# Performance work log

Hardware: AMD Instinct MI355X
Metric: run time of the kernel (lower is better)

Reference implementation:

```python
import jax, jax.numpy as jnp
import numpy as np

D, H, WIN, OUT = 3, 64, 8, 32
B, T = 128, 129
IU, JU = np.triu_indices(D, k=1)  # Lyndon pairs i<j at depth 2


def setup_inputs() -> dict:
    key = jax.random.key(0)
    ks = jax.random.split(key, 10)
    ts = jnp.broadcast_to(jnp.linspace(0.0, 1.0, T), (B, T))
    # path-like control values: cumulative sum of small increments
    x = jnp.cumsum(0.1 * jax.random.normal(ks[0], (B, T, D)), axis=1)
    def lin(k, o, i):
        return jax.random.normal(k, (o, i), dtype=jnp.float32) * (1.0 / np.sqrt(i))
    return {
        "ts": ts, "x": x,
        "W0": lin(ks[1], 128, D), "b0": jnp.zeros((128,), jnp.float32),
        "W1": lin(ks[2], 128, 128), "b1": jnp.zeros((128,), jnp.float32),
        "W2": lin(ks[3], H, 128), "b2": jnp.zeros((H,), jnp.float32),
        "V0": lin(ks[4], 128, H), "c0": jnp.zeros((128,), jnp.float32),
        "V1": lin(ks[5], 128, 128), "c1": jnp.zeros((128,), jnp.float32),
        "V2": lin(ks[6], D * H, 128), "c2": jnp.zeros((D * H,), jnp.float32),
        "R": lin(ks[7], OUT, H), "rb": jnp.zeros((OUT,), jnp.float32),
    }


def reference(ts, x, W0, b0, W1, b1, W2, b2, V0, c0, V1, c1, V2, c2, R, rb):
    sp = jax.nn.softplus

    def init_mlp(v):  # R^D -> R^H, Euclidean retract = identity
        return W2 @ sp(W1 @ sp(W0 @ v + b0) + b1) + b2

    def vf_flat(y):  # R^H -> R^{D*H}, final tanh (split_multi_vector_field)
        return jnp.tanh(V2 @ sp(V1 @ sp(V0 @ y + c0) + c1) + c2)

    def F(y):
        # level-1 fields f_i(y) as rows of m: (D, H)
        m = vf_flat(y).reshape(D, H)
        # J[a, b] = D f_b(y) . f_a(y)  via JVPs in directions f_a
        J = jax.vmap(lambda v: jax.jvp(vf_flat, (y,), (v,))[1].reshape(D, H))(m)
        # Lyndon level-2 brackets [f_i, f_j] = Df_j.f_i - Df_i.f_j
        br = J[IU, JU] - J[JU, IU]  # (D*(D-1)/2, H)
        return jnp.concatenate([m, br], axis=0).T  # (H, logsig_size)

    def logsigs_fn(xs):  # depth-2 log-signatures over disjoint windows
        nw = (T - 1) // WIN
        idx = (np.arange(nw) * WIN)[:, None] + np.arange(WIN + 1)[None, :]
        win = xs[idx]
        lvl1 = win[:, -1] - win[:, 0]       # increments
        rel = win[:, :-1] - win[:, :1]      # path relative to window start
        dv = win[:, 1:] - win[:, :-1]       # increments within window
        a = jnp.einsum('nki,nkj->nij', rel, dv)
        area = 0.5 * (a - jnp.swapaxes(a, 1, 2))  # Levy areas
        return jnp.concatenate([lvl1, area[:, IU, JU]], axis=1)

    def solve_one(t, xs):
        h0 = init_mlp(xs[0])
        ls = logsigs_fn(xs)                       # (nw, L)
        t_sig = t[::WIN]                          # window knot times
        slopes = ls / (t_sig[1:] - t_sig[:-1])[:, None]  # dz/dt per window
        slope_steps = jnp.repeat(slopes, WIN, axis=0)    # (T-1, L)
        dts = t[1:] - t[:-1]

        def step(y, inp):  # Heun integration of dy = F(y) dz/dt dt
            dt, s = inp
            k1 = F(y) @ s
            k2 = F(y + dt * k1) @ s
            yn = y + 0.5 * dt * (k1 + k2)
            return yn, yn

        _, ys = jax.lax.scan(step, h0, (dts, slope_steps))
        hidden = jnp.concatenate([h0[None], ys], axis=0)  # (T, H)
        return jnp.tanh(hidden @ R.T + rb)                # evolving readout

    return jax.vmap(solve_one)(ts, x)  # (B, T, OUT)
```

## Files before the change

### kernel.cpp

```cpp
#include <hip/hip_runtime.h>
#include <math.h>

#define BB 128
#define TT 129
#define NSTEP 128
#define NW 16
#define WINW 8
#define OUTD 32

typedef _Float16 h2_t __attribute__((ext_vector_type(2)));

__device__ __forceinline__ float fast_rcp(float v){ return __builtin_amdgcn_rcpf(v); }
__device__ __forceinline__ float tanh_f(float v){
    float ax=fminf(fabsf(v),15.f); float e=__expf(2.f*ax);
    float r=1.f-2.f*fast_rcp(e+1.f); return copysignf(r,v);
}
__device__ __forceinline__ void sigsp(float z, float& sp, float& sig){
    float e  = __expf(-fabsf(z));
    float rc = fast_rcp(1.f+e);
    sp  = fmaxf(z,0.f) + __logf(1.f+e);
    sig = (z>=0.f) ? rc : e*rc;
}
__device__ __forceinline__ float pack2(float a,float b){
    h2_t h; h.x=(_Float16)a; h.y=(_Float16)b; return __builtin_bit_cast(float,h);
}
__device__ __forceinline__ float dot2c(float wc,float ac,float acc){
    return __builtin_amdgcn_fdot2(__builtin_bit_cast(h2_t,wc),__builtin_bit_cast(h2_t,ac),acc,false);
}
__device__ __forceinline__ float dot2q(float4 wq,float4 aq,float acc){
    acc=dot2c(wq.x,aq.x,acc); acc=dot2c(wq.y,aq.y,acc);
    acc=dot2c(wq.z,aq.z,acc); acc=dot2c(wq.w,aq.w,acc); return acc;
}
#define DOT4(acc,Wv,Av) acc += (Wv).x*(Av).x + (Wv).y*(Av).y + (Wv).z*(Av).z + (Wv).w*(Av).w
#define PIN4(v) asm volatile("" : "+v"((v).x), "+v"((v).y), "+v"((v).z), "+v"((v).w))

#define DPPF(x,ctrl) __builtin_bit_cast(float, __builtin_amdgcn_update_dpp(0, __builtin_bit_cast(int,(x)), (ctrl), 0xF, 0xF, true))
__device__ __forceinline__ float dpp_xor1(float x){ return DPPF(x,0xB1); }
__device__ __forceinline__ float dpp_xor2(float x){ return DPPF(x,0x4E); }
__device__ __forceinline__ float dpp_hmir(float x){ return DPPF(x,0x141); }
#define RED4(x) do{ x += dpp_xor1(x); x += dpp_xor2(x); }while(0)

__global__ __launch_bounds__(512, 1)
void ncde_solve(const float* __restrict__ ts, const float* __restrict__ x,
                const float* __restrict__ W0, const float* __restrict__ b0,
                const float* __restrict__ W1, const float* __restrict__ b1,
                const float* __restrict__ W2, const float* __restrict__ b2,
                const float* __restrict__ V0, const float* __restrict__ c0,
                const float* __restrict__ V1, const float* __restrict__ c1,
                const float* __restrict__ V2, const float* __restrict__ c2,
                const float* __restrict__ R, const float* __restrict__ rb,
                float* __restrict__ out)
{
    const int b = blockIdx.x;
    const int t = threadIdx.x;
    const int r = t >> 2, q = t & 3;
    const int rl = r & 63;
    const int pt = (t >= 256) ? (t - 256) : 0;
    const int prow = pt >> 3, poct = pt & 7;

    __shared__ __align__(16) float RSh[OUTD*68];
    __shared__ __align__(16) float ySh[64];
    __shared__ __align__(16) float yp[32], y2p[32];
    __shared__ __align__(16) float a0H[64], a1H[64];
    __shared__ __align__(16) float mpH[96];
    __shared__ __align__(16) float u0H[192], wH[192];
    __shared__ float mF32[64];
    __shared__ float slopesSh[NW][6];
    __shared__ float dtsSh[NSTEP];

    float4 v0c[2], v1c[4], v2c[3][4];
    {
        auto pkld = [](const float* src)->float4{
            const float4* p=(const float4*)src;
            float4 a=p[0], c=p[1];
            float4 rr; rr.x=pack2(a.x,a.y); rr.y=pack2(a.z,a.w); rr.z=pack2(c.x,c.y); rr.w=pack2(c.z,c.w);
            return rr;
        };
        {
            const float* base = V0 + r*64 + q*16;
            v0c[0]=pkld(base); v0c[1]=pkld(base+8);
        }
        {
            const float* base = V1 + r*128 + q*32;
            #pragma unroll
            for (int k=0;k<4;k++) v1c[k]=pkld(base+8*k);
        }
        #pragma unroll
        for (int i=0;i<3;i++){
            const float* base = V2 + (rl+64*i)*128 + q*32;
            #pragma unroll
            for (int k=0;k<4;k++) v2c[i][k]=pkld(base+8*k);
        }
        PIN4(v0c[0]); PIN4(v0c[1]);
        #pragma unroll
        for (int k=0;k<4;k++) PIN4(v1c[k]);
        #pragma unroll
        for (int i=0;i<3;i++){
            #pragma unroll
            for (int k=0;k<4;k++) PIN4(v2c[i][k]);
        }
    }
    const float c0r=c0[r], c1r=c1[r];
    const float c2a=c2[rl], c2b=c2[64+rl], c2c=c2[128+rl];
    const float rbp = rb[prow & 31];

    for (int i=t; i<OUTD*64; i+=512) RSh[(i>>6)*68 + (i&63)] = R[i];
    const float* tsb = ts + (size_t)b*TT;
    if (t < NSTEP) dtsSh[t] = tsb[t+1] - tsb[t];

    if (t < NW) {
        const int w = t;
        const float* xs = x + (size_t)(b*TT + w*WINW)*3;
        float x0c[3] = {xs[0], xs[1], xs[2]};
        float prev[3] = {x0c[0], x0c[1], x0c[2]};
        float am01=0.f, am02=0.f, am12=0.f, am10=0.f, am20=0.f, am21=0.f;
        #pragma unroll
        for (int k=0;k<WINW;k++) {
            float cur[3] = {xs[(k+1)*3+0], xs[(k+1)*3+1], xs[(k+1)*3+2]};
            float rel[3], dv[3];
            #pragma unroll
            for (int c=0;c<3;c++){ rel[c]=prev[c]-x0c[c]; dv[c]=cur[c]-prev[c]; }
            am01 += rel[0]*dv[1]; am10 += rel[1]*dv[0];
            am02 += rel[0]*dv[2]; am20 += rel[2]*dv[0];
            am12 += rel[1]*dv[2]; am21 += rel[2]*dv[1];
            prev[0]=cur[0]; prev[1]=cur[1]; prev[2]=cur[2];
        }
        const float invden = 1.f/(tsb[(w+1)*WINW] - tsb[w*WINW]);
        slopesSh[w][0] = (prev[0]-x0c[0])*invden;
        slopesSh[w][1] = (prev[1]-x0c[1])*invden;
        slopesSh[w][2] = (prev[2]-x0c[2])*invden;
        slopesSh[w][3] = 0.5f*(am01-am10)*invden;
        slopesSh[w][4] = 0.5f*(am02-am20)*invden;
        slopesSh[w][5] = 0.5f*(am12-am21)*invden;
    }

    if (t < 128) {
        const float xv0 = x[(size_t)b*TT*3+0];
        const float xv1 = x[(size_t)b*TT*3+1];
        const float xv2 = x[(size_t)b*TT*3+2];
        float acc = b0[t] + W0[t*3]*xv0 + W0[t*3+1]*xv1 + W0[t*3+2]*xv2;
        float sp, sg; sigsp(acc, sp, sg);
        u0H[t] = sp;
    }
    __syncthreads();
    if (t < 128) {
        float acc = b1[t];
        const float4* rw = (const float4*)(W1 + t*128);
        #pragma unroll 8
        for (int k=0;k<32;k++){ float4 wv=rw[k]; float4 av=*(const float4*)&u0H[4*k]; DOT4(acc,wv,av); }
        float sp, sg; sigsp(acc, sp, sg);
        wH[t] = sp;
    }
    __syncthreads();
    if (t < 64) {
        float acc = b2[t];
        const float4* rw = (const float4*)(W2 + t*128);
        #pragma unroll 8
        for (int k=0;k<32;k++){ float4 wv=rw[k]; float4 av=*(const float4*)&wH[4*k]; DOT4(acc,wv,av); }
        ySh[t] = acc;
        ((_Float16*)yp)[t] = (_Float16)acc;
    }
    __syncthreads();

    float yreg = (r < 64) ? ySh[r] : 0.f;
    float k1r = 0.f;
    float S0,S1,S2,S3,S4,S5;

    auto Feval = [&](const float* ypIn, bool first, float dtc) {
        float sig0r, sig1r, mA=0.f, mC=0.f;
        {
            const float4* Y = (const float4*)ypIn;
            float za = dot2q(v0c[0], Y[q*2], 0.f);
            float zb = dot2q(v0c[1], Y[q*2+1], 0.f);
            float z = za + zb;
            RED4(z); z += c0r;
            float sp; sigsp(z, sp, sig0r);
            if (!q) ((_Float16*)a0H)[r] = (_Float16)sp;
        }
        __syncthreads();
        {
            const float4* A = (const float4*)a0H + q*4;
            float za = dot2q(v1c[0], A[0], 0.f); za = dot2q(v1c[1], A[1], za);
            float zb = dot2q(v1c[2], A[2], 0.f); zb = dot2q(v1c[3], A[3], zb);
            float z = za + zb;
            RED4(z); z += c1r;
            float sp; sigsp(z, sp, sig1r);
            if (!q) ((_Float16*)a1H)[r] = (_Float16)sp;
        }
        __syncthreads();
        {
            const float4* A = (const float4*)a1H + q*4;
            float4 a0=A[0],a1=A[1],a2=A[2],a3=A[3];
            if (r < 64){
                float zAa=dot2q(v2c[0][0],a0,0.f); zAa=dot2q(v2c[0][1],a1,zAa);
                float zAb=dot2q(v2c[0][2],a2,0.f); zAb=dot2q(v2c[0][3],a3,zAb);
                float zCa=dot2q(v2c[2][0],a0,0.f); zCa=dot2q(v2c[2][1],a1,zCa);
                float zCb=dot2q(v2c[2][2],a2,0.f); zCb=dot2q(v2c[2][3],a3,zCb);
                float zA=zAa+zAb, zC=zCa+zCb;
                RED4(zA); RED4(zC);
                mA = tanh_f(zA + c2a); mC = tanh_f(zC + c2c);
                if (!q){
                    ((_Float16*)mpH)[rl]     = (_Float16)mA;
                    ((_Float16*)mpH)[128+rl] = (_Float16)mC;
                }
            } else {
                float zBa=dot2q(v2c[1][0],a0,0.f); zBa=dot2q(v2c[1][1],a1,zBa);
                float zBb=dot2q(v2c[1][2],a2,0.f); zBb=dot2q(v2c[1][3],a3,zBb);
                float zB=zBa+zBb;
                RED4(zB);
                float mB = tanh_f(zB + c2b);
                if (!q){
                    ((_Float16*)mpH)[64+rl] = (_Float16)mB;
                    mF32[rl] = mB;
                }
            }
        }
        __syncthreads();
        {
            const float4* M = (const float4*)mpH;
            float4 g0a=M[q*2],    g0b=M[q*2+1];
            float4 g1a=M[8+q*2],  g1b=M[8+q*2+1];
            float4 g2a=M[16+q*2], g2b=M[16+q*2+1];
            float t0=dot2q(v0c[0],g0a,0.f); t0=dot2q(v0c[1],g0b,t0);
            float t1=dot2q(v0c[0],g1a,0.f); t1=dot2q(v0c[1],g1b,t1);
            float t2=dot2q(v0c[0],g2a,0.f); t2=dot2q(v0c[1],g2b,t2);
            RED4(t0); RED4(t1); RED4(t2);
            if (!q){
                ((_Float16*)u0H)[r]     = (_Float16)(sig0r*t0);
                ((_Float16*)u0H)[128+r] = (_Float16)(sig0r*t1);
                ((_Float16*)u0H)[256+r] = (_Float16)(sig0r*t2);
            }
        }
        __syncthreads();
        {
            const float4* U = (const float4*)u0H;
            float t0a=0.f,t0b=0.f,t1a=0.f,t1b=0.f,t2a=0.f,t2b=0.f;
            #pragma unroll
            for (int k=0;k<2;k++){
                float4 w = v1c[k];
                t0a=dot2q(w,U[q*4+k],t0a); t1a=dot2q(w,U[16+q*4+k],t1a); t2a=dot2q(w,U[32+q*4+k],t2a);
            }
            #pragma unroll
            for (int k=2;k<4;k++){
                float4 w = v1c[k];
                t0b=dot2q(w,U[q*4+k],t0b); t1b=dot2q(w,U[16+q*4+k],t1b); t2b=dot2q(w,U[32+q*4+k],t2b);
            }
            float t0=t0a+t0b, t1=t1a+t1b, t2=t2a+t2b;
            RED4(t0); RED4(t1); RED4(t2);
            if (!q){
                float w0 = sig1r*(S3*t1 + S4*t2);
                float w1 = sig1r*(S3*t0 - S5*t2);
                float w2 = sig1r*(S4*t0 + S5*t1);
                ((_Float16*)wH)[r]     = (_Float16)w0;
                ((_Float16*)wH)[128+r] = (_Float16)w1;
                ((_Float16*)wH)[256+r] = (_Float16)w2;
            }
        }
        __syncthreads();
        if (r < 64){
            const float4* W = (const float4*)wH;
            float D0a=dot2q(v2c[0][0],W[q*4+0],0.f);   D0a=dot2q(v2c[0][1],W[q*4+1],D0a);
            float D0b=dot2q(v2c[0][2],W[q*4+2],0.f);   D0b=dot2q(v2c[0][3],W[q*4+3],D0b);
            float D1a=dot2q(v2c[1][0],W[16+q*4+0],0.f);D1a=dot2q(v2c[1][1],W[16+q*4+1],D1a);
            float D1b=dot2q(v2c[1][2],W[16+q*4+2],0.f);D1b=dot2q(v2c[1][3],W[16+q*4+3],D1b);
            float D2a=dot2q(v2c[2][0],W[32+q*4+0],0.f);D2a=dot2q(v2c[2][1],W[32+q*4+1],D2a);
            float D2b=dot2q(v2c[2][2],W[32+q*4+2],0.f);D2b=dot2q(v2c[2][3],W[32+q*4+3],D2b);
            float D0=D0a+D0b, D1=D1a+D1b, D2=D2a+D2b;
            RED4(D0); RED4(D1); RED4(D2);
            const float mB = mF32[rl];
            const float dtA = 1.f-mA*mA, dtB = 1.f-mB*mB, dtC = 1.f-mC*mC;
            float kk = mA*S0 + mB*S1 + mC*S2 - dtA*D0 + dtB*D1 + dtC*D2;
            if (first){
                k1r = kk;
                float y2 = yreg + dtc*kk;
                if (!q) ((_Float16*)y2p)[rl] = (_Float16)y2;
            } else {
                yreg += 0.5f*dtc*(k1r + kk);
                if (!q){ ((_Float16*)yp)[rl] = (_Float16)yreg; ySh[rl] = yreg; }
            }
        }
        __syncthreads();
    };

    auto proj = [&](int stp) {
        if (t >= 256){
            const float4* rr = (const float4*)(RSh + prow*68 + poct*8);
            const float4* yy = (const float4*)(ySh + poct*8);
            float pacc = 0.f;
            DOT4(pacc, rr[0], yy[0]); DOT4(pacc, rr[1], yy[1]);
            pacc += dpp_xor1(pacc);
            pacc += dpp_xor2(pacc);
            pacc += dpp_hmir(pacc);
            if (!poct) out[(size_t)(b*TT + stp)*OUTD + prow] = tanh_f(pacc + rbp);
        }
    };

    for (int step=0; step<NSTEP; ++step) {
        proj(step);
        const int w = step >> 3;
        S0=slopesSh[w][0]; S1=slopesSh[w][1]; S2=slopesSh[w][2];
        S3=slopesSh[w][3]; S4=slopesSh[w][4]; S5=slopesSh[w][5];
        const float dtc = dtsSh[step];
        Feval(yp,  true,  dtc);
        Feval(y2p, false, dtc);
    }
    proj(NSTEP);
}

extern "C" void kernel_launch(void* const* d_in, const int* in_sizes, int n_in,
                              void* d_out, int out_size, void* d_ws, size_t ws_size,
                              hipStream_t stream) {
    const float* ts = (const float*)d_in[0];
    const float* x  = (const float*)d_in[1];
    const float* W0 = (const float*)d_in[2];
    const float* b0 = (const float*)d_in[3];
    const float* W1 = (const float*)d_in[4];
    const float* b1 = (const float*)d_in[5];
    const float* W2 = (const float*)d_in[6];
    const float* b2 = (const float*)d_in[7];
    const float* V0 = (const float*)d_in[8];
    const float* c0 = (const float*)d_in[9];
    const float* V1 = (const float*)d_in[10];
    const float* c1 = (const float*)d_in[11];
    const float* V2 = (const float*)d_in[12];
    const float* c2 = (const float*)d_in[13];
    const float* R  = (const float*)d_in[14];
    const float* rb = (const float*)d_in[15];
    float* out = (float*)d_out;

    ncde_solve<<<dim3(BB), dim3(512), 0, stream>>>(
        ts, x, W0, b0, W1, b1, W2, b2, V0, c0, V1, c1, V2, c2, R, rb, out);
}
```

Baseline: 590.9 us.

## Halve block to 256 threads, each quad computing two hidden rows

Shrinks each block from 512 to 256 threads. Each 4-lane group now owns two rows of the 128-wide layers and all three rows of the output layer, so the weight slices kept in registers double. The goal is to drop the idle half-block branches in the output and JVP stages and to make the many per-step barriers cheaper with fewer waves to synchronise. The cost is more register pressure and more serial dot-product work per thread, with only 128 blocks on the device.

```diff
diff --git a/kernel.cpp b/kernel.cpp
--- a/kernel.cpp
+++ b/kernel.cpp
@@ -40,7 +40,7 @@
 __device__ __forceinline__ float dpp_hmir(float x){ return DPPF(x,0x141); }
 #define RED4(x) do{ x += dpp_xor1(x); x += dpp_xor2(x); }while(0)
 
-__global__ __launch_bounds__(512, 1)
+__global__ __launch_bounds__(256, 1)
 void ncde_solve(const float* __restrict__ ts, const float* __restrict__ x,
                 const float* __restrict__ W0, const float* __restrict__ b0,
                 const float* __restrict__ W1, const float* __restrict__ b1,
@@ -54,9 +54,7 @@
     const int b = blockIdx.x;
     const int t = threadIdx.x;
     const int r = t >> 2, q = t & 3;
-    const int rl = r & 63;
-    const int pt = (t >= 256) ? (t - 256) : 0;
-    const int prow = pt >> 3, poct = pt & 7;
+    const int prow = t >> 3, poct = t & 7;
 
     __shared__ __align__(16) float RSh[OUTD*68];
     __shared__ __align__(16) float ySh[64];
@@ -64,11 +62,10 @@
     __shared__ __align__(16) float a0H[64], a1H[64];
     __shared__ __align__(16) float mpH[96];
     __shared__ __align__(16) float u0H[192], wH[192];
-    __shared__ float mF32[64];
     __shared__ float slopesSh[NW][6];
     __shared__ float dtsSh[NSTEP];
 
-    float4 v0c[2], v1c[4], v2c[3][4];
+    float4 v0c[2][2], v1c[2][4], v2c[3][4];
     {
         auto pkld = [](const float* src)->float4{
             const float4* p=(const float4*)src;
@@ -76,35 +73,42 @@
             float4 rr; rr.x=pack2(a.x,a.y); rr.y=pack2(a.z,a.w); rr.z=pack2(c.x,c.y); rr.w=pack2(c.z,c.w);
             return rr;
         };
-        {
-            const float* base = V0 + r*64 + q*16;
-            v0c[0]=pkld(base); v0c[1]=pkld(base+8);
-        }
-        {
-            const float* base = V1 + r*128 + q*32;
-            #pragma unroll
-            for (int k=0;k<4;k++) v1c[k]=pkld(base+8*k);
+        #pragma unroll
+        for (int i=0;i<2;i++){
+            const float* base = V0 + (r+64*i)*64 + q*16;
+            v0c[i][0]=pkld(base); v0c[i][1]=pkld(base+8);
+        }
+        #pragma unroll
+        for (int i=0;i<2;i++){
+            const float* base = V1 + (r+64*i)*128 + q*32;
+            #pragma unroll
+            for (int k=0;k<4;k++) v1c[i][k]=pkld(base+8*k);
         }
         #pragma unroll
         for (int i=0;i<3;i++){
-            const float* base = V2 + (rl+64*i)*128 + q*32;
+            const float* base = V2 + (r+64*i)*128 + q*32;
             #pragma unroll
             for (int k=0;k<4;k++) v2c[i][k]=pkld(base+8*k);
         }
-        PIN4(v0c[0]); PIN4(v0c[1]);
-        #pragma unroll
-        for (int k=0;k<4;k++) PIN4(v1c[k]);
+        #pragma unroll
+        for (int i=0;i<2;i++){ PIN4(v0c[i][0]); PIN4(v0c[i][1]); }
+        #pragma unroll
+        for (int i=0;i<2;i++){
+            #pragma unroll
+            for (int k=0;k<4;k++) PIN4(v1c[i][k]);
+        }
         #pragma unroll
         for (int i=0;i<3;i++){
             #pragma unroll
             for (int k=0;k<4;k++) PIN4(v2c[i][k]);
         }
     }
-    const float c0r=c0[r], c1r=c1[r];
-    const float c2a=c2[rl], c2b=c2[64+rl], c2c=c2[128+rl];
+    const float c0A=c0[r], c0B=c0[64+r];
+    const float c1A=c1[r], c1B=c1[64+r];
+    const float c2a=c2[r], c2b=c2[64+r], c2c=c2[128+r];
     const float rbp = rb[prow & 31];
 
-    for (int i=t; i<OUTD*64; i+=512) RSh[(i>>6)*68 + (i&63)] = R[i];
+    for (int i=t; i<OUTD*64; i+=256) RSh[(i>>6)*68 + (i&63)] = R[i];
     const float* tsb = ts + (size_t)b*TT;
     if (t < NSTEP) dtsSh[t] = tsb[t+1] - tsb[t];
 
@@ -162,57 +166,62 @@
     }
     __syncthreads();
 
-    float yreg = (r < 64) ? ySh[r] : 0.f;
+    float yreg = ySh[r];
     float k1r = 0.f;
     float S0,S1,S2,S3,S4,S5;
 
     auto Feval = [&](const float* ypIn, bool first, float dtc) {
-        float sig0r, sig1r, mA=0.f, mC=0.f;
+        float sig0A,sig0B,sig1A,sig1B,mA,mB,mC,dtA,dtB,dtC;
         {
             const float4* Y = (const float4*)ypIn;
-            float za = dot2q(v0c[0], Y[q*2], 0.f);
-            float zb = dot2q(v0c[1], Y[q*2+1], 0.f);
-            float z = za + zb;
-            RED4(z); z += c0r;
-            float sp; sigsp(z, sp, sig0r);
-            if (!q) ((_Float16*)a0H)[r] = (_Float16)sp;
+            float4 y0=Y[q*2], y1=Y[q*2+1];
+            float zA = dot2q(v0c[0][0],y0,0.f); zA = dot2q(v0c[0][1],y1,zA);
+            float zB = dot2q(v0c[1][0],y0,0.f); zB = dot2q(v0c[1][1],y1,zB);
+            RED4(zA); RED4(zB);
+            zA += c0A; zB += c0B;
+            float spA, spB;
+            sigsp(zA, spA, sig0A); sigsp(zB, spB, sig0B);
+            if (!q){
+                ((_Float16*)a0H)[r]    = (_Float16)spA;
+                ((_Float16*)a0H)[64+r] = (_Float16)spB;
+            }
         }
         __syncthreads();
         {
             const float4* A = (const float4*)a0H + q*4;
-            float za = dot2q(v1c[0], A[0], 0.f); za = dot2q(v1c[1], A[1], za);
-            float zb = dot2q(v1c[2], A[2], 0.f); zb = dot2q(v1c[3], A[3], zb);
-            float z = za + zb;
-            RED4(z); z += c1r;
-            float sp; sigsp(z, sp, sig1r);
-            if (!q) ((_Float16*)a1H)[r] = (_Float16)sp;
+            float4 a0=A[0],a1=A[1],a2=A[2],a3=A[3];
+            float zAa=dot2q(v1c[0][0],a0,0.f); zAa=dot2q(v1c[0][1],a1,zAa);
+            float zAb=dot2q(v1c[0][2],a2,0.f); zAb=dot2q(v1c[0][3],a3,zAb);
+            float zBa=dot2q(v1c[1][0],a0,0.f); zBa=dot2q(v1c[1][1],a1,zBa);
+            float zBb=dot2q(v1c[1][2],a2,0.f); zBb=dot2q(v1c[1][3],a3,zBb);
+            float zA=zAa+zAb, zB=zBa+zBb;
+            RED4(zA); RED4(zB);
+            zA += c1A; zB += c1B;
+            float spA, spB;
+            sigsp(zA, spA, sig1A); sigsp(zB, spB, sig1B);
+            if (!q){
+                ((_Float16*)a1H)[r]    = (_Float16)spA;
+                ((_Float16*)a1H)[64+r] = (_Float16)spB;
+            }
         }
         __syncthreads();
         {
             const float4* A = (const float4*)a1H + q*4;
             float4 a0=A[0],a1=A[1],a2=A[2],a3=A[3];
-            if (r < 64){
-                float zAa=dot2q(v2c[0][0],a0,0.f); zAa=dot2q(v2c[0][1],a1,zAa);
-                float zAb=dot2q(v2c[0][2],a2,0.f); zAb=dot2q(v2c[0][3],a3,zAb);
-                float zCa=dot2q(v2c[2][0],a0,0.f); zCa=dot2q(v2c[2][1],a1,zCa);
-                float zCb=dot2q(v2c[2][2],a2,0.f); zCb=dot2q(v2c[2][3],a3,zCb);
-                float zA=zAa+zAb, zC=zCa+zCb;
-                RED4(zA); RED4(zC);
-                mA = tanh_f(zA + c2a); mC = tanh_f(zC + c2c);
-                if (!q){
-                    ((_Float16*)mpH)[rl]     = (_Float16)mA;
-                    ((_Float16*)mpH)[128+rl] = (_Float16)mC;
-                }
-            } else {
-                float zBa=dot2q(v2c[1][0],a0,0.f); zBa=dot2q(v2c[1][1],a1,zBa);
-                float zBb=dot2q(v2c[1][2],a2,0.f); zBb=dot2q(v2c[1][3],a3,zBb);
-                float zB=zBa+zBb;
-                RED4(zB);
-                float mB = tanh_f(zB + c2b);
-                if (!q){
-                    ((_Float16*)mpH)[64+rl] = (_Float16)mB;
-                    mF32[rl] = mB;
-                }
+            float zAa=dot2q(v2c[0][0],a0,0.f); zAa=dot2q(v2c[0][1],a1,zAa);
+            float zAb=dot2q(v2c[0][2],a2,0.f); zAb=dot2q(v2c[0][3],a3,zAb);
+            float zBa=dot2q(v2c[1][0],a0,0.f); zBa=dot2q(v2c[1][1],a1,zBa);
+            float zBb=dot2q(v2c[1][2],a2,0.f); zBb=dot2q(v2c[1][3],a3,zBb);
+            float zCa=dot2q(v2c[2][0],a0,0.f); zCa=dot2q(v2c[2][1],a1,zCa);
+            float zCb=dot2q(v2c[2][2],a2,0.f); zCb=dot2q(v2c[2][3],a3,zCb);
+            float zA=zAa+zAb, zB=zBa+zBb, zC=zCa+zCb;
+            RED4(zA); RED4(zB); RED4(zC);
+            mA=tanh_f(zA+c2a); mB=tanh_f(zB+c2b); mC=tanh_f(zC+c2c);
+            dtA=1.f-mA*mA; dtB=1.f-mB*mB; dtC=1.f-mC*mC;
+            if (!q){
+                ((_Float16*)mpH)[r]     = (_Float16)mA;
+                ((_Float16*)mpH)[64+r]  = (_Float16)mB;
+                ((_Float16*)mpH)[128+r] = (_Float16)mC;
             }
         }
         __syncthreads();
@@ -221,43 +230,57 @@
             float4 g0a=M[q*2],    g0b=M[q*2+1];
             float4 g1a=M[8+q*2],  g1b=M[8+q*2+1];
             float4 g2a=M[16+q*2], g2b=M[16+q*2+1];
-            float t0=dot2q(v0c[0],g0a,0.f); t0=dot2q(v0c[1],g0b,t0);
-            float t1=dot2q(v0c[0],g1a,0.f); t1=dot2q(v0c[1],g1b,t1);
-            float t2=dot2q(v0c[0],g2a,0.f); t2=dot2q(v0c[1],g2b,t2);
-            RED4(t0); RED4(t1); RED4(t2);
-            if (!q){
-                ((_Float16*)u0H)[r]     = (_Float16)(sig0r*t0);
-                ((_Float16*)u0H)[128+r] = (_Float16)(sig0r*t1);
-                ((_Float16*)u0H)[256+r] = (_Float16)(sig0r*t2);
+            float t0A=dot2q(v0c[0][0],g0a,0.f); t0A=dot2q(v0c[0][1],g0b,t0A);
+            float t1A=dot2q(v0c[0][0],g1a,0.f); t1A=dot2q(v0c[0][1],g1b,t1A);
+            float t2A=dot2q(v0c[0][0],g2a,0.f); t2A=dot2q(v0c[0][1],g2b,t2A);
+            float t0B=dot2q(v0c[1][0],g0a,0.f); t0B=dot2q(v0c[1][1],g0b,t0B);
+            float t1B=dot2q(v0c[1][0],g1a,0.f); t1B=dot2q(v0c[1][1],g1b,t1B);
+            float t2B=dot2q(v0c[1][0],g2a,0.f); t2B=dot2q(v0c[1][1],g2b,t2B);
+            RED4(t0A); RED4(t1A); RED4(t2A);
+            RED4(t0B); RED4(t1B); RED4(t2B);
+            if (!q){
+                ((_Float16*)u0H)[r]      = (_Float16)(sig0A*t0A);
+                ((_Float16*)u0H)[64+r]   = (_Float16)(sig0B*t0B);
+                ((_Float16*)u0H)[128+r]  = (_Float16)(sig0A*t1A);
+                ((_Float16*)u0H)[192+r]  = (_Float16)(sig0B*t1B);
+                ((_Float16*)u0H)[256+r]  = (_Float16)(sig0A*t2A);
+                ((_Float16*)u0H)[320+r]  = (_Float16)(sig0B*t2B);
             }
         }
         __syncthreads();
         {
             const float4* U = (const float4*)u0H;
-            float t0a=0.f,t0b=0.f,t1a=0.f,t1b=0.f,t2a=0.f,t2b=0.f;
+            float t0Aa=0.f,t0Ab=0.f,t1Aa=0.f,t1Ab=0.f,t2Aa=0.f,t2Ab=0.f;
+            float t0Ba=0.f,t0Bb=0.f,t1Ba=0.f,t1Bb=0.f,t2Ba=0.f,t2Bb=0.f;
             #pragma unroll
             for (int k=0;k<2;k++){
-                float4 w = v1c[k];
-                t0a=dot2q(w,U[q*4+k],t0a); t1a=dot2q(w,U[16+q*4+k],t1a); t2a=dot2q(w,U[32+q*4+k],t2a);
+                float4 wa=v1c[0][k], wb=v1c[1][k];
+                float4 g0=U[q*4+k], g1=U[16+q*4+k], g2=U[32+q*4+k];
+                t0Aa=dot2q(wa,g0,t0Aa); t1Aa=dot2q(wa,g1,t1Aa); t2Aa=dot2q(wa,g2,t2Aa);
+                t0Ba=dot2q(wb,g0,t0Ba); t1Ba=dot2q(wb,g1,t1Ba); t2Ba=dot2q(wb,g2,t2Ba);
             }
             #pragma unroll
             for (int k=2;k<4;k++){
-                float4 w = v1c[k];
-                t0b=dot2q(w,U[q*4+k],t0b); t1b=dot2q(w,U[16+q*4+k],t1b); t2b=dot2q(w,U[32+q*4+k],t2b);
-            }
-            float t0=t0a+t0b, t1=t1a+t1b, t2=t2a+t2b;
-            RED4(t0); RED4(t1); RED4(t2);
-            if (!q){
-                float w0 = sig1r*(S3*t1 + S4*t2);
-                float w1 = sig1r*(S3*t0 - S5*t2);
-                float w2 = sig1r*(S4*t0 + S5*t1);
-                ((_Float16*)wH)[r]     = (_Float16)w0;
-                ((_Float16*)wH)[128+r] = (_Float16)w1;
-                ((_Float16*)wH)[256+r] = (_Float16)w2;
-            }
-        }
-        __syncthreads();
-        if (r < 64){
+                float4 wa=v1c[0][k], wb=v1c[1][k];
+                float4 g0=U[q*4+k], g1=U[16+q*4+k], g2=U[32+q*4+k];
+                t0Ab=dot2q(wa,g0,t0Ab); t1Ab=dot2q(wa,g1,t1Ab); t2Ab=dot2q(wa,g2,t2Ab);
+                t0Bb=dot2q(wb,g0,t0Bb); t1Bb=dot2q(wb,g1,t1Bb); t2Bb=dot2q(wb,g2,t2Bb);
+            }
+            float t0A=t0Aa+t0Ab, t1A=t1Aa+t1Ab, t2A=t2Aa+t2Ab;
+            float t0B=t0Ba+t0Bb, t1B=t1Ba+t1Bb, t2B=t2Ba+t2Bb;
+            RED4(t0A); RED4(t1A); RED4(t2A);
+            RED4(t0B); RED4(t1B); RED4(t2B);
+            if (!q){
+                ((_Float16*)wH)[r]      = (_Float16)(sig1A*(S3*t1A + S4*t2A));
+                ((_Float16*)wH)[64+r]   = (_Float16)(sig1B*(S3*t1B + S4*t2B));
+                ((_Float16*)wH)[128+r]  = (_Float16)(sig1A*(S3*t0A - S5*t2A));
+                ((_Float16*)wH)[192+r]  = (_Float16)(sig1B*(S3*t0B - S5*t2B));
+                ((_Float16*)wH)[256+r]  = (_Float16)(sig1A*(S4*t0A + S5*t1A));
+                ((_Float16*)wH)[320+r]  = (_Float16)(sig1B*(S4*t0B + S5*t1B));
+            }
+        }
+        __syncthreads();
+        {
             const float4* W = (const float4*)wH;
             float D0a=dot2q(v2c[0][0],W[q*4+0],0.f);   D0a=dot2q(v2c[0][1],W[q*4+1],D0a);
             float D0b=dot2q(v2c[0][2],W[q*4+2],0.f);   D0b=dot2q(v2c[0][3],W[q*4+3],D0b);
@@ -267,32 +290,28 @@
             float D2b=dot2q(v2c[2][2],W[32+q*4+2],0.f);D2b=dot2q(v2c[2][3],W[32+q*4+3],D2b);
             float D0=D0a+D0b, D1=D1a+D1b, D2=D2a+D2b;
             RED4(D0); RED4(D1); RED4(D2);
-            const float mB = mF32[rl];
-            const float dtA = 1.f-mA*mA, dtB = 1.f-mB*mB, dtC = 1.f-mC*mC;
             float kk = mA*S0 + mB*S1 + mC*S2 - dtA*D0 + dtB*D1 + dtC*D2;
             if (first){
                 k1r = kk;
                 float y2 = yreg + dtc*kk;
-                if (!q) ((_Float16*)y2p)[rl] = (_Float16)y2;
+                if (!q) ((_Float16*)y2p)[r] = (_Float16)y2;
             } else {
                 yreg += 0.5f*dtc*(k1r + kk);
-                if (!q){ ((_Float16*)yp)[rl] = (_Float16)yreg; ySh[rl] = yreg; }
+                if (!q){ ((_Float16*)yp)[r] = (_Float16)yreg; ySh[r] = yreg; }
             }
         }
         __syncthreads();
     };
 
     auto proj = [&](int stp) {
-        if (t >= 256){
-            const float4* rr = (const float4*)(RSh + prow*68 + poct*8);
-            const float4* yy = (const float4*)(ySh + poct*8);
-            float pacc = 0.f;
-            DOT4(pacc, rr[0], yy[0]); DOT4(pacc, rr[1], yy[1]);
-            pacc += dpp_xor1(pacc);
-            pacc += dpp_xor2(pacc);
-            pacc += dpp_hmir(pacc);
-            if (!poct) out[(size_t)(b*TT + stp)*OUTD + prow] = tanh_f(pacc + rbp);
-        }
+        const float4* rr = (const float4*)(RSh + prow*68 + poct*8);
+        const float4* yy = (const float4*)(ySh + poct*8);
+        float pacc = 0.f;
+        DOT4(pacc, rr[0], yy[0]); DOT4(pacc, rr[1], yy[1]);
+        pacc += dpp_xor1(pacc);
+        pacc += dpp_xor2(pacc);
+        pacc += dpp_hmir(pacc);
+        if (!poct) out[(size_t)(b*TT + stp)*OUTD + prow] = tanh_f(pacc + rbp);
     };
 
     for (int step=0; step<NSTEP; ++step) {
@@ -328,6 +347,6 @@
     const float* rb = (const float*)d_in[15];
     float* out = (float*)d_out;
 
-    ncde_solve<<<dim3(BB), dim3(512), 0, stream>>>(
+    ncde_solve<<<dim3(BB), dim3(256), 0, stream>>>(
         ts, x, W0, b0, W1, b1, W2, b2, V0, c0, V1, c1, V2, c2, R, rb, out);
 }
```

After: 589.3 us. About the same (-0.3%).
